# Performance work log

Measured on AMD Instinct MI355X. Metric: run time of the kernel, lower is better.

The kernel has to match this reference:

```python
import jax, jax.numpy as jnp
import numpy as np

B, T, IN, H, L, OUT = 128, 1024, 256, 512, 2, 256


def setup_inputs() -> dict:
    key = jax.random.key(0)
    ks = jax.random.split(key, 12)
    s_in = 1.0 / np.sqrt(H)  # torch RNNCell init scale (uniform +-1/sqrt(H))
    u = lambda k, shape: jax.random.uniform(k, shape, jnp.float32, -s_in, s_in)
    return {
        "x": jax.random.normal(ks[0], (B, T, IN), jnp.float32),
        "h0": jnp.zeros((L, B, H), jnp.float32),
        "w_ih0": u(ks[1], (H, IN)),
        "w_hh0": u(ks[2], (H, H)),
        "b_ih0": u(ks[3], (H,)),
        "b_hh0": u(ks[4], (H,)),
        "w_ih1": u(ks[5], (H, H)),
        "w_hh1": u(ks[6], (H, H)),
        "b_ih1": u(ks[7], (H,)),
        "b_hh1": u(ks[8], (H,)),
        "fc_w": u(ks[9], (OUT, H)),
        "fc_b": u(ks[10], (OUT,)),
    }


def reference(x, h0, w_ih0, w_hh0, b_ih0, b_hh0, w_ih1, w_hh1, b_ih1, b_hh1, fc_w, fc_b):
    # x: [B, T, IN] -> scan over time axis
    xt = jnp.swapaxes(x, 0, 1)  # [T, B, IN]

    def step(hs, x_t):
        h0_, h1_ = hs
        h0n = jnp.tanh(x_t @ w_ih0.T + b_ih0 + h0_ @ w_hh0.T + b_hh0)
        h1n = jnp.tanh(h0n @ w_ih1.T + b_ih1 + h1_ @ w_hh1.T + b_hh1)
        return (h0n, h1n), None

    (h0f, h1f), _ = jax.lax.scan(step, (h0[0], h0[1]), xt)
    # original: out = outs[-1].squeeze(); fc(out). squeeze is a no-op for B>1.
    return h1f @ fc_w.T + fc_b
```

## Files before the change

### kernel.cpp

```cpp
#include <hip/hip_runtime.h>

#define BB   128
#define TT   1024
#define INP  256
#define HH   512
#define OUTD 256
#define GB   16
#define NG   8
#define NBLK 256

typedef float  f32x4  __attribute__((ext_vector_type(4)));
typedef short  short8 __attribute__((ext_vector_type(8)));
typedef unsigned long long u64;

__device__ __forceinline__ unsigned short bf16_rne(float f) {
  union { float f; unsigned u; } v; v.f = f;
  unsigned r = v.u + 0x7fffu + ((v.u >> 16) & 1u);
  return (unsigned short)(r >> 16);
}

__device__ __forceinline__ float fast_tanh(float x) {
  float t = __builtin_amdgcn_exp2f(x * 2.8853900817779268f);
  return 1.0f - 2.0f * __builtin_amdgcn_rcpf(t + 1.0f);
}

__device__ __forceinline__ short8 pack8(f32x4 a, f32x4 b) {
  union { unsigned short s[8]; short8 v; } u;
  u.s[0] = bf16_rne(a[0]); u.s[1] = bf16_rne(a[1]);
  u.s[2] = bf16_rne(a[2]); u.s[3] = bf16_rne(a[3]);
  u.s[4] = bf16_rne(b[0]); u.s[5] = bf16_rne(b[1]);
  u.s[6] = bf16_rne(b[2]); u.s[7] = bf16_rne(b[3]);
  return u.v;
}

__device__ __forceinline__ short8 load_cvt8(const float* p) {
  const f32x4* q = (const f32x4*)p;
  return pack8(q[0], q[1]);
}

__device__ __forceinline__ f32x4 ntload4(const float* p) {
  return __builtin_nontemporal_load((const f32x4*)p);
}

__device__ __forceinline__ short8 l2load8(const unsigned short* p) {
  union { u64 q[2]; short8 v; } u;
  const u64* pp = (const u64*)p;
  u.q[0] = __hip_atomic_load(pp,     __ATOMIC_RELAXED, __HIP_MEMORY_SCOPE_AGENT);
  u.q[1] = __hip_atomic_load(pp + 1, __ATOMIC_RELAXED, __HIP_MEMORY_SCOPE_AGENT);
  return u.v;
}

__device__ __forceinline__ unsigned short* hslot(unsigned short* base, int slot, int g) {
  return base + ((size_t)(slot * NG + g)) * (16 * 64 * 8);
}

__global__ void __launch_bounds__(256, 1) rnn_mfma(
    const float* __restrict__ x,
    const float* __restrict__ h0init,
    const float* __restrict__ w_ih0,
    const float* __restrict__ w_hh0,
    const float* __restrict__ b_ih0,
    const float* __restrict__ b_hh0,
    const float* __restrict__ w_ih1,
    const float* __restrict__ w_hh1,
    const float* __restrict__ b_ih1,
    const float* __restrict__ b_hh1,
    const float* __restrict__ fc_w,
    const float* __restrict__ fc_b,
    float* __restrict__ out,
    unsigned* __restrict__ ws_ctl,
    unsigned short* __restrict__ h0f,
    unsigned short* __restrict__ h1f)
{
  extern __shared__ char lds_pad[];
  (void)lds_pad;
  const int tid = threadIdx.x;

  __shared__ unsigned sh_tk, sh_g;
  if (tid == 0) {
    unsigned xcc;
    asm volatile("s_getreg_b32 %0, hwreg(HW_REG_XCC_ID)" : "=s"(xcc));
    xcc &= 7;
    sh_g  = xcc;
    sh_tk = __hip_atomic_fetch_add(ws_ctl + xcc * 32, 1u,
                                   __ATOMIC_RELAXED, __HIP_MEMORY_SCOPE_AGENT);
  }
  __syncthreads();
  const unsigned ticket = sh_tk;
  const int g = (int)sh_g;
  if (ticket >= 16) return;

  const int role = (int)ticket;
  const bool isL0 = role < 8;
  const int wv   = tid >> 6;
  const int lane = tid & 63;
  const int ln   = lane & 15;
  const int q    = lane >> 4;
  const int j0   = (role & 7) * 64 + wv * 16 + ln;
  const int jq   = (role & 7) * 64 + wv * 16 + q * 4;
  const int bg   = g * GB;

  volatile int* flags  = (volatile int*)(ws_ctl + 1024 + g * 512);
  volatile int* myflag = flags + role * 32;

  for (int c = tid; c < 2048; c += 256) {
    int a  = c >> 10;
    int bl = (c >> 6) & 15;
    int j8 = (c & 63) * 8;
    short8 v = load_cvt8(h0init + ((size_t)a * BB + (bg + bl)) * HH + j8);
    unsigned short* dst = hslot(a ? h1f : h0f, 3, g)
        + ((size_t)((j8 >> 5) * 64 + ((j8 >> 3) & 3) * 16 + bl)) * 8;
    *(short8*)dst = v;
  }
  __syncthreads();
  if (tid == 0) *myflag = 1;

  short8 Bf0[24];
  short8 Bf1[32];
  if (isL0) {
#pragma unroll
    for (int kb = 0; kb < 24; ++kb) {
      int k = kb * 32 + q * 8;
      const float* src = (k < INP) ? (w_ih0 + (size_t)j0 * INP + k)
                                   : (w_hh0 + (size_t)j0 * HH + (k - INP));
      Bf0[kb] = load_cvt8(src);
    }
  } else {
#pragma unroll
    for (int kb = 0; kb < 32; ++kb) {
      int k = kb * 32 + q * 8;
      const float* src = (k < HH) ? (w_ih1 + (size_t)j0 * HH + k)
                                  : (w_hh1 + (size_t)j0 * HH + (k - HH));
      Bf1[kb] = load_cvt8(src);
    }
  }
  f32x4 bias4;
  {
    const float* bi = isL0 ? b_ih0 : b_ih1;
    const float* bh = isL0 ? b_hh0 : b_hh1;
    bias4 = *(const f32x4*)(bi + jq) + *(const f32x4*)(bh + jq);
  }

  short8 xa[8];
  if (isL0) {
    const float* xp = x + ((size_t)(bg + ln) * TT + 0) * INP;
#pragma unroll
    for (int kb = 0; kb < 8; ++kb)
      xa[kb] = pack8(ntload4(xp + kb * 32 + q * 8), ntload4(xp + kb * 32 + q * 8 + 4));
  }

  const f32x4 z = {0.f, 0.f, 0.f, 0.f};
  const int tmax = isL0 ? (TT - 1) : TT;

#pragma unroll 1
  for (int t = 0; t <= tmax; ++t) {
    if (isL0) {
      f32x4 xr[16];
      const bool havex = (t + 1 < TT);
      if (havex) {
        const float* xp = x + ((size_t)(bg + ln) * TT + (t + 1)) * INP;
#pragma unroll
        for (int kb = 0; kb < 8; ++kb) {
          xr[2 * kb]     = ntload4(xp + kb * 32 + q * 8);
          xr[2 * kb + 1] = ntload4(xp + kb * 32 + q * 8 + 4);
        }
      }

      {
        volatile int* fp = flags + (lane & 15) * 32;
        const int thr = ((lane & 15) < 8) ? (t + 1) : (t - 1);
        while (!__all(*fp >= thr)) {}
        asm volatile("" ::: "memory");
      }

      const unsigned short* hp0 = hslot(h0f, (t + 3) & 3, g);
      short8 Af[16];
#pragma unroll
      for (int kb = 0; kb < 16; ++kb)
        Af[kb] = l2load8(hp0 + ((size_t)kb * 64 + lane) * 8);

      f32x4 ac[4] = {z, z, z, z};
#pragma unroll
      for (int kb = 0; kb < 8; ++kb)
        ac[kb & 3] = __builtin_amdgcn_mfma_f32_16x16x32_bf16(
            Bf0[kb], xa[kb], ac[kb & 3], 0, 0, 0);
#pragma unroll
      for (int kb = 8; kb < 24; ++kb)
        ac[kb & 3] = __builtin_amdgcn_mfma_f32_16x16x32_bf16(
            Bf0[kb], Af[kb - 8], ac[kb & 3], 0, 0, 0);

      f32x4 d = ac[0] + ac[1] + ac[2] + ac[3];
      unsigned short* wdst = hslot(h0f, t & 3, g);
      union { unsigned short s[4]; u64 q8; } uu;
#pragma unroll
      for (int r = 0; r < 4; ++r)
        uu.s[r] = bf16_rne(fast_tanh(d[r] + bias4[r]));
      *(u64*)(wdst + (size_t)((jq >> 5) * 64 + ((jq >> 3) & 3) * 16 + ln) * 8
              + (jq & 7)) = uu.q8;
      if (havex) {
#pragma unroll
        for (int kb = 0; kb < 8; ++kb)
          xa[kb] = pack8(xr[2 * kb], xr[2 * kb + 1]);
      }
    } else {
      {
        volatile int* fp = flags + (8 + (lane & 7)) * 32;
        while (!__all(*fp >= t + 1)) {}
        asm volatile("" ::: "memory");
      }
      const unsigned short* hp1 = hslot(h1f, (t + 2) & 3, g);
      short8 Af1[16];
#pragma unroll
      for (int kb = 0; kb < 16; ++kb)
        Af1[kb] = l2load8(hp1 + ((size_t)kb * 64 + lane) * 8);

      {
        volatile int* fp = flags + (lane & 7) * 32;
        while (!__all(*fp >= t + 1)) {}
        asm volatile("" ::: "memory");
      }

      if (t >= 1) {
        const unsigned short* hp0 = hslot(h0f, (t + 3) & 3, g);
        short8 Af0[16];
#pragma unroll
        for (int kb = 0; kb < 16; ++kb)
          Af0[kb] = l2load8(hp0 + ((size_t)kb * 64 + lane) * 8);

        f32x4 ac[4] = {z, z, z, z};
#pragma unroll
        for (int kb = 0; kb < 16; ++kb)
          ac[kb & 3] = __builtin_amdgcn_mfma_f32_16x16x32_bf16(
              Bf1[kb + 16], Af1[kb], ac[kb & 3], 0, 0, 0);
#pragma unroll
        for (int kb = 0; kb < 16; ++kb)
          ac[kb & 3] = __builtin_amdgcn_mfma_f32_16x16x32_bf16(
              Bf1[kb], Af0[kb], ac[kb & 3], 0, 0, 0);

        f32x4 d = ac[0] + ac[1] + ac[2] + ac[3];
        unsigned short* wdst = hslot(h1f, (t + 3) & 3, g);
        union { unsigned short s[4]; u64 q8; } uu;
#pragma unroll
        for (int r = 0; r < 4; ++r)
          uu.s[r] = bf16_rne(fast_tanh(d[r] + bias4[r]));
        *(u64*)(wdst + (size_t)((jq >> 5) * 64 + ((jq >> 3) & 3) * 16 + ln) * 8
                + (jq & 7)) = uu.q8;
      }
    }

    __syncthreads();
    if (tid == 0) *myflag = t + 2;
  }

  if (tid < 16) {
    volatile int* fp = flags + tid * 32;
    const int thr = (tid < 8) ? (TT + 1) : (TT + 2);
    while (*fp < thr) {}
  }
  __syncthreads();

  if (wv == 0) {
    const unsigned short* hp = hslot(h1f, 3, g);
    const int o_ln = role * 16 + ln;
    const int o_q  = role * 16 + q * 4;
    f32x4 ac[4] = {z, z, z, z};
#pragma unroll
    for (int kb = 0; kb < 16; ++kb) {
      int k = kb * 32 + q * 8;
      short8 Bfc = load_cvt8(fc_w + (size_t)o_ln * HH + k);
      short8 Af  = l2load8(hp + ((size_t)kb * 64 + lane) * 8);
      ac[kb & 3] = __builtin_amdgcn_mfma_f32_16x16x32_bf16(
          Bfc, Af, ac[kb & 3], 0, 0, 0);
    }
    f32x4 fb = *(const f32x4*)(fc_b + o_q);
    f32x4 v = ac[0] + ac[1] + ac[2] + ac[3] + fb;
    *(f32x4*)(out + (size_t)(bg + ln) * OUTD + o_q) = v;
  }
}

extern "C" void kernel_launch(void* const* d_in, const int* in_sizes, int n_in,
                              void* d_out, int out_size, void* d_ws, size_t ws_size,
                              hipStream_t stream) {
  (void)in_sizes; (void)n_in; (void)out_size; (void)ws_size;

  const float* x      = (const float*)d_in[0];
  const float* h0init = (const float*)d_in[1];
  const float* w_ih0  = (const float*)d_in[2];
  const float* w_hh0  = (const float*)d_in[3];
  const float* b_ih0  = (const float*)d_in[4];
  const float* b_hh0  = (const float*)d_in[5];
  const float* w_ih1  = (const float*)d_in[6];
  const float* w_hh1  = (const float*)d_in[7];
  const float* b_ih1  = (const float*)d_in[8];
  const float* b_hh1  = (const float*)d_in[9];
  const float* fc_w   = (const float*)d_in[10];
  const float* fc_b   = (const float*)d_in[11];
  float* out = (float*)d_out;

  unsigned* ws_ctl = (unsigned*)d_ws;
  unsigned short* h0f = (unsigned short*)((char*)d_ws + 32768);
  unsigned short* h1f = h0f + 4 * NG * (16 * 64 * 8);

  hipMemsetAsync(d_ws, 0, 32768, stream);

  rnn_mfma<<<dim3(NBLK), dim3(256), 90112, stream>>>(
      x, h0init, w_ih0, w_hh0, b_ih0, b_hh0, w_ih1, w_hh1, b_ih1, b_hh1,
      fc_w, fc_b, out, ws_ctl, h0f, h1f);
}
```

Baseline: 4.312 ms.

## Replace per-block barrier with per-wavefront flags and reorder x prefetch

Each wavefront now publishes its own progress flag, so the per-step __syncthreads and block-level flag are removed and consumers poll 32 per-wave flags instead of 8 per-block ones. Layer-0 waves publish their h slice before loading the next x timestep, putting the flag write earlier on the critical path. Pollers sleep briefly between checks, and layer 1 skips loading h1 at t=0. This enlarges the control region and adds more polling traffic, and it loses the overlap of the x load with the flag wait.

```diff
diff --git a/kernel.cpp b/kernel.cpp
--- a/kernel.cpp
+++ b/kernel.cpp
@@ -100,8 +100,9 @@
   const int jq   = (role & 7) * 64 + wv * 16 + q * 4;
   const int bg   = g * GB;
 
-  volatile int* flags  = (volatile int*)(ws_ctl + 1024 + g * 512);
-  volatile int* myflag = flags + role * 32;
+  volatile int* flags  = (volatile int*)(ws_ctl + 1024 + g * 2048);
+  const int myline = isL0 ? (role * 4 + wv) : (32 + (role - 8) * 4 + wv);
+  volatile int* myflag = flags + myline * 32;
 
   for (int c = tid; c < 2048; c += 256) {
     int a  = c >> 10;
@@ -113,7 +114,7 @@
     *(short8*)dst = v;
   }
   __syncthreads();
-  if (tid == 0) *myflag = 1;
+  if (lane == 0) *myflag = 1;
 
   short8 Bf0[24];
   short8 Bf1[32];
@@ -155,21 +156,10 @@
 #pragma unroll 1
   for (int t = 0; t <= tmax; ++t) {
     if (isL0) {
-      f32x4 xr[16];
-      const bool havex = (t + 1 < TT);
-      if (havex) {
-        const float* xp = x + ((size_t)(bg + ln) * TT + (t + 1)) * INP;
-#pragma unroll
-        for (int kb = 0; kb < 8; ++kb) {
-          xr[2 * kb]     = ntload4(xp + kb * 32 + q * 8);
-          xr[2 * kb + 1] = ntload4(xp + kb * 32 + q * 8 + 4);
-        }
-      }
-
       {
-        volatile int* fp = flags + (lane & 15) * 32;
-        const int thr = ((lane & 15) < 8) ? (t + 1) : (t - 1);
-        while (!__all(*fp >= thr)) {}
+        volatile int* fp = flags + lane * 32;
+        const int thr = (lane < 32) ? (t + 1) : (t - 1);
+        while (!__all(*fp >= thr)) __builtin_amdgcn_s_sleep(1);
         asm volatile("" ::: "memory");
       }
 
@@ -197,26 +187,33 @@
         uu.s[r] = bf16_rne(fast_tanh(d[r] + bias4[r]));
       *(u64*)(wdst + (size_t)((jq >> 5) * 64 + ((jq >> 3) & 3) * 16 + ln) * 8
               + (jq & 7)) = uu.q8;
-      if (havex) {
+      asm volatile("s_waitcnt vmcnt(0)" ::: "memory");
+      if (lane == 0) *myflag = t + 2;
+      __builtin_amdgcn_sched_barrier(0);
+
+      if (t + 1 < TT) {
+        const float* xp = x + ((size_t)(bg + ln) * TT + (t + 1)) * INP;
 #pragma unroll
         for (int kb = 0; kb < 8; ++kb)
-          xa[kb] = pack8(xr[2 * kb], xr[2 * kb + 1]);
+          xa[kb] = pack8(ntload4(xp + kb * 32 + q * 8),
+                         ntload4(xp + kb * 32 + q * 8 + 4));
       }
     } else {
       {
-        volatile int* fp = flags + (8 + (lane & 7)) * 32;
-        while (!__all(*fp >= t + 1)) {}
+        volatile int* fp = flags + (32 + (lane & 31)) * 32;
+        while (!__all(*fp >= t + 1)) __builtin_amdgcn_s_sleep(1);
         asm volatile("" ::: "memory");
       }
-      const unsigned short* hp1 = hslot(h1f, (t + 2) & 3, g);
       short8 Af1[16];
-#pragma unroll
-      for (int kb = 0; kb < 16; ++kb)
-        Af1[kb] = l2load8(hp1 + ((size_t)kb * 64 + lane) * 8);
-
+      if (t >= 1) {
+        const unsigned short* hp1 = hslot(h1f, (t + 2) & 3, g);
+#pragma unroll
+        for (int kb = 0; kb < 16; ++kb)
+          Af1[kb] = l2load8(hp1 + ((size_t)kb * 64 + lane) * 8);
+      }
       {
-        volatile int* fp = flags + (lane & 7) * 32;
-        while (!__all(*fp >= t + 1)) {}
+        volatile int* fp = flags + (lane & 31) * 32;
+        while (!__all(*fp >= t + 1)) __builtin_amdgcn_s_sleep(1);
         asm volatile("" ::: "memory");
       }
 
@@ -246,20 +243,17 @@
         *(u64*)(wdst + (size_t)((jq >> 5) * 64 + ((jq >> 3) & 3) * 16 + ln) * 8
                 + (jq & 7)) = uu.q8;
       }
-    }
-
-    __syncthreads();
-    if (tid == 0) *myflag = t + 2;
-  }
-
-  if (tid < 16) {
-    volatile int* fp = flags + tid * 32;
-    const int thr = (tid < 8) ? (TT + 1) : (TT + 2);
-    while (*fp < thr) {}
-  }
-  __syncthreads();
+      asm volatile("s_waitcnt vmcnt(0)" ::: "memory");
+      if (lane == 0) *myflag = t + 2;
+    }
+  }
 
   if (wv == 0) {
+    {
+      volatile int* fp = flags + (32 + (lane & 31)) * 32;
+      while (!__all(*fp >= TT + 2)) {}
+      asm volatile("" ::: "memory");
+    }
     const unsigned short* hp = hslot(h1f, 3, g);
     const int o_ln = role * 16 + ln;
     const int o_q  = role * 16 + q * 4;
@@ -298,10 +292,10 @@
   float* out = (float*)d_out;
 
   unsigned* ws_ctl = (unsigned*)d_ws;
-  unsigned short* h0f = (unsigned short*)((char*)d_ws + 32768);
+  unsigned short* h0f = (unsigned short*)((char*)d_ws + 131072);
   unsigned short* h1f = h0f + 4 * NG * (16 * 64 * 8);
 
-  hipMemsetAsync(d_ws, 0, 32768, stream);
+  hipMemsetAsync(d_ws, 0, 131072, stream);
 
   rnn_mfma<<<dim3(NBLK), dim3(256), 90112, stream>>>(
       x, h0init, w_ih0, w_hh0, b_ih0, b_hh0, w_ih1, w_hh1, b_ih1, b_hh1,
```

After: 6.322 ms. 46.6% more time.
